# Performance work log

Hardware: AMD Instinct MI355X
Metric: run time of the kernel (lower is better)

The kernel has to match this reference:

```python
import jax, jax.numpy as jnp
import numpy as np

N_NODES = 100000
N_EDGES = 1600000
IN_DIM, HID_DIM, OUT_DIM = 128, 128, 64


def gcn_conv(x, W, b, src, dst, edge_weight, n_nodes):
    """PyG GCNConv: symmetric norm with self-loops (weight 1.0), x@W, scatter-add, +bias."""
    xw = x @ W                                   # [N, out]
    deg = jax.ops.segment_sum(edge_weight, dst, num_segments=n_nodes) + 1.0  # self-loop weight 1
    dis = jnp.where(deg > 0, jax.lax.rsqrt(deg), 0.0)       # deg^{-1/2}
    norm = dis[src] * edge_weight * dis[dst]                # per-edge norm
    agg = jax.ops.segment_sum(norm[:, None] * xw[src], dst, num_segments=n_nodes)
    self_term = (dis * dis)[:, None] * xw                   # self-loop contribution
    return agg + self_term + b


def setup_inputs() -> dict:
    key = jax.random.key(0)
    ks = jax.random.split(key, 12)
    x = jax.random.normal(ks[0], (N_NODES, IN_DIM), dtype=jnp.float32)
    edge_index = jax.random.randint(ks[1], (2, N_EDGES), 0, N_NODES, dtype=jnp.int64 if jax.config.jax_enable_x64 else jnp.int32)
    edge_curvature = jax.random.normal(ks[2], (N_EDGES, 1), dtype=jnp.float32)
    s = 0.1
    W1 = jax.random.normal(ks[3], (IN_DIM, HID_DIM), dtype=jnp.float32) * s
    b1 = jnp.zeros((HID_DIM,), dtype=jnp.float32)
    W2 = jax.random.normal(ks[4], (HID_DIM, OUT_DIM), dtype=jnp.float32) * s
    b2 = jnp.zeros((OUT_DIM,), dtype=jnp.float32)
    mw1 = jax.random.normal(ks[5], (1, 16), dtype=jnp.float32) * s
    mb1 = jnp.zeros((16,), dtype=jnp.float32)
    mw2 = jax.random.normal(ks[6], (16, 1), dtype=jnp.float32) * s
    mb2 = jnp.zeros((1,), dtype=jnp.float32)
    return {"x": x, "edge_index": edge_index, "edge_curvature": edge_curvature,
            "W1": W1, "b1": b1, "W2": W2, "b2": b2,
            "mw1": mw1, "mb1": mb1, "mw2": mw2, "mb2": mb2}


def reference(x, edge_index, edge_curvature, W1, b1, W2, b2, mw1, mb1, mw2, mb2):
    src, dst = edge_index[0], edge_index[1]
    # curv_mlp: Linear(1,16) -> ReLU -> Linear(16,1) -> Sigmoid
    h = jax.nn.relu(edge_curvature @ mw1 + mb1)
    w = jax.nn.sigmoid(h @ mw2 + mb2)[:, 0]
    edge_weight = 0.1 + 0.9 * w
    h1 = jax.nn.relu(gcn_conv(x, W1, b1, src, dst, edge_weight, N_NODES))
    # dropout p=0.5 is identity in eval mode
    out = gcn_conv(h1, W2, b2, src, dst, edge_weight, N_NODES)
    return out
```

## Files before the change

### kernel.cpp

```cpp
#include <hip/hip_runtime.h>


constexpr int N_NODES = 100000;
constexpr int N_EDGES = 1600000;
constexpr int IN_DIM  = 128;
constexpr int HID_DIM = 128;
constexpr int OUT_DIM = 64;

constexpr int RANGE = 256;
constexpr int NBUK  = (N_NODES + RANGE - 1) / RANGE;
constexpr int EPB   = 8192;
constexpr int NPART = (N_EDGES + EPB - 1) / EPB;
constexpr int STAGE_CAP = 6144;

using bf16x8 = __attribute__((ext_vector_type(8))) short;
using f32x4  = __attribute__((ext_vector_type(4))) float;

__device__ __forceinline__ unsigned short f2b(float f)
{
    unsigned int u = __float_as_uint(f);
    u += 0x7fffu + ((u >> 16) & 1u);
    return (unsigned short)(u >> 16);
}

__device__ __forceinline__ float edge_weight_mlp(float c,
                                                 const float* __restrict__ mw1,
                                                 const float* __restrict__ mb1,
                                                 const float* __restrict__ mw2,
                                                 const float* __restrict__ mb2)
{
    float z = mb2[0];
#pragma unroll
    for (int i = 0; i < 16; ++i) {
        float h = fmaf(c, mw1[i], mb1[i]);
        h = fmaxf(h, 0.0f);
        z = fmaf(h, mw2[i], z);
    }
    float s = 1.0f / (1.0f + __expf(-z));
    return fmaf(0.9f, s, 0.1f);
}

__global__ __launch_bounds__(512) void k_hist(const int* __restrict__ dst,
                                              int* __restrict__ blockHist,
                                              int* __restrict__ gcnt)
{
    __shared__ int hist[NBUK];
    const int tid = threadIdx.x;
    const int b   = blockIdx.x;
    for (int i = tid; i < NBUK; i += 512) hist[i] = 0;
    __syncthreads();
    const int base = b * EPB;
    const int n = min(EPB, N_EDGES - base);
    for (int i = tid; i < n; i += 512)
        atomicAdd(&hist[dst[base + i] >> 8], 1);
    __syncthreads();
    for (int i = tid; i < NBUK; i += 512) {
        int h = hist[i];
        blockHist[(size_t)i * NPART + b] = h;
        if (h) atomicAdd(&gcnt[i], h);
    }
}

__global__ __launch_bounds__(512) void k_scan_buckets(const int* __restrict__ gcnt,
                                                      int* __restrict__ bucketBase)
{
    __shared__ int sm[512];
    const int t = threadIdx.x;
    int v = (t < NBUK) ? gcnt[t] : 0;
    sm[t] = v;
    __syncthreads();
#pragma unroll
    for (int o = 1; o < 512; o <<= 1) {
        int u = (t >= o) ? sm[t - o] : 0;
        __syncthreads();
        sm[t] += u;
        __syncthreads();
    }
    if (t < NBUK) bucketBase[t] = sm[t] - v;
    if (t == NBUK - 1) bucketBase[NBUK] = sm[t];
}

__global__ __launch_bounds__(256) void k_colscan(int* __restrict__ blockHist,
                                                 const int* __restrict__ bucketBase)
{
    const int j = blockIdx.x;
    const int t = threadIdx.x;
    __shared__ int sm[256];
    int v = (t < NPART) ? blockHist[(size_t)j * NPART + t] : 0;
    sm[t] = v;
    __syncthreads();
#pragma unroll
    for (int o = 1; o < 256; o <<= 1) {
        int u = (t >= o) ? sm[t - o] : 0;
        __syncthreads();
        sm[t] += u;
        __syncthreads();
    }
    if (t < NPART)
        blockHist[(size_t)j * NPART + t] = bucketBase[j] + sm[t] - v;
}

__global__ __launch_bounds__(512) void k_partition(const float* __restrict__ curv,
                                                   const int*   __restrict__ src,
                                                   const int*   __restrict__ dst,
                                                   const float* __restrict__ mw1,
                                                   const float* __restrict__ mb1,
                                                   const float* __restrict__ mw2,
                                                   const float* __restrict__ mb2,
                                                   const int*   __restrict__ blockHist,
                                                   int2* __restrict__ ep_tmp)
{
    __shared__ int cur[NBUK];
    const int tid = threadIdx.x;
    const int b   = blockIdx.x;
    for (int i = tid; i < NBUK; i += 512)
        cur[i] = blockHist[(size_t)i * NPART + b];
    __syncthreads();
    const int base = b * EPB;
    const int n = min(EPB, N_EDGES - base);
    for (int i = tid; i < n; i += 512) {
        int e = base + i;
        int d = dst[e];
        float w = edge_weight_mlp(curv[e], mw1, mb1, mw2, mb2);
        int pos = atomicAdd(&cur[d >> 8], 1);
        int meta = src[e] | ((d & (RANGE - 1)) << 17);
        ep_tmp[pos] = make_int2(meta, __float_as_int(w));
    }
}

__global__ __launch_bounds__(256) void k_bucket_sort(const int2* __restrict__ ep_tmp,
                                                     const int*  __restrict__ bucketBase,
                                                     int2* __restrict__ ep,
                                                     int*  __restrict__ rp,
                                                     float* __restrict__ dis)
{
    const int b   = blockIdx.x;
    const int tid = threadIdx.x;
    const int base  = bucketBase[b];
    const int nE    = bucketBase[b + 1] - base;
    const int node0 = b * RANGE;
    const int nNodes = min(RANGE, N_NODES - node0);

    __shared__ int2  stage[STAGE_CAP];
    __shared__ int   cnt[RANGE];
    __shared__ float deg[RANGE];
    __shared__ int   sm[RANGE];
    __shared__ int   cur[RANGE];

    const bool fit = (nE <= STAGE_CAP);

    cnt[tid] = 0;
    deg[tid] = 0.0f;
    __syncthreads();
    for (int i = tid; i < nE; i += 256) {
        int2 t = ep_tmp[base + i];
        if (fit) stage[i] = t;
        int dl = (t.x >> 17) & (RANGE - 1);
        atomicAdd(&cnt[dl], 1);
        atomicAdd(&deg[dl], __int_as_float(t.y));
    }
    __syncthreads();
    int c = cnt[tid];
    sm[tid] = c;
    __syncthreads();
#pragma unroll
    for (int o = 1; o < 256; o <<= 1) {
        int u = (tid >= o) ? sm[tid - o] : 0;
        __syncthreads();
        sm[tid] += u;
        __syncthreads();
    }
    int excl = sm[tid] - c;
    cur[tid] = base + excl;
    if (tid < nNodes) {
        rp[node0 + tid]  = base + excl;
        dis[node0 + tid] = rsqrtf(deg[tid] + 1.0f);
    }
    if (b == NBUK - 1 && tid == 0) rp[N_NODES] = N_EDGES;
    __syncthreads();
    for (int i = tid; i < nE; i += 256) {
        int2 t = fit ? stage[i] : ep_tmp[base + i];
        int dl = (t.x >> 17) & (RANGE - 1);
        int pos = atomicAdd(&cur[dl], 1);
        ep[pos] = make_int2(t.x & 0x1FFFF, t.y);
    }
}

template <int KIN, int KOUT>
__global__ __launch_bounds__(256) void k_prepack(const float* __restrict__ W,
                                                 unsigned short* __restrict__ wp)
{
    constexpr int KS = KIN / 32;
    constexpr int NSLOT = (KOUT / 16) * KS * 64;
    int idx = blockIdx.x * blockDim.x + threadIdx.x;
    if (idx >= NSLOT) return;
    int l  = idx & 63;
    int t  = idx >> 6;
    int ks = t % KS;
    int nt = t / KS;
    int col = nt * 16 + (l & 15);
    int k0  = ks * 32 + (l >> 4) * 8;
    unsigned short o[8];
#pragma unroll
    for (int j = 0; j < 8; ++j)
        o[j] = f2b(W[(k0 + j) * KOUT + col]);
    *reinterpret_cast<uint4*>(&wp[(size_t)idx * 8]) = *reinterpret_cast<uint4*>(o);
}

template <int KIN, int KOUT, bool AFP32>
__global__ __launch_bounds__(256) void k_gemm_mfma(const void* __restrict__ Aptr,
                                                   const unsigned short* __restrict__ Wp,
                                                   const float* __restrict__ dis,
                                                   unsigned short* __restrict__ C)
{
    constexpr int NT = KOUT / 16;
    constexpr int KS = KIN / 32;
    const int tid  = threadIdx.x;
    const int lane = tid & 63;
    const int wave = blockIdx.x * (blockDim.x >> 6) + (tid >> 6);
    const int row0 = wave * 16;
    if (row0 >= N_NODES) return;

    f32x4 acc[NT];
#pragma unroll
    for (int nt = 0; nt < NT; ++nt)
        acc[nt] = f32x4{0.f, 0.f, 0.f, 0.f};

    const int arow = row0 + (lane & 15);
    const int koff = (lane >> 4) * 8;
#pragma unroll
    for (int ks = 0; ks < KS; ++ks) {
        bf16x8 a;
        if constexpr (AFP32) {
            const float* A = (const float*)Aptr;
            const float* p = A + (size_t)arow * KIN + ks * 32 + koff;
            float4 f0 = *reinterpret_cast<const float4*>(p);
            float4 f1 = *reinterpret_cast<const float4*>(p + 4);
            a[0] = (short)f2b(f0.x); a[1] = (short)f2b(f0.y);
            a[2] = (short)f2b(f0.z); a[3] = (short)f2b(f0.w);
            a[4] = (short)f2b(f1.x); a[5] = (short)f2b(f1.y);
            a[6] = (short)f2b(f1.z); a[7] = (short)f2b(f1.w);
        } else {
            const unsigned short* A = (const unsigned short*)Aptr;
            a = *reinterpret_cast<const bf16x8*>(A + (size_t)arow * KIN + ks * 32 + koff);
        }
#pragma unroll
        for (int nt = 0; nt < NT; ++nt) {
            bf16x8 bfr = *reinterpret_cast<const bf16x8*>(Wp + ((size_t)(nt * KS + ks) * 64 + lane) * 8);
            acc[nt] = __builtin_amdgcn_mfma_f32_16x16x32_bf16(a, bfr, acc[nt], 0, 0, 0);
        }
    }

    const int r0 = row0 + ((lane >> 4) << 2);
    const int c0 = lane & 15;
    float dv[4];
#pragma unroll
    for (int r = 0; r < 4; ++r) dv[r] = dis[r0 + r];
#pragma unroll
    for (int nt = 0; nt < NT; ++nt) {
#pragma unroll
        for (int r = 0; r < 4; ++r)
            C[(size_t)(r0 + r) * KOUT + nt * 16 + c0] = f2b(acc[nt][r] * dv[r]);
    }
}

template <int DIM, bool RELU, bool OBF16>
__global__ __launch_bounds__(256) void k_gather(const int*  __restrict__ rp,
                                                const int2* __restrict__ ep,
                                                const unsigned short* __restrict__ xws,
                                                const float* __restrict__ dis,
                                                const float* __restrict__ bias,
                                                void* __restrict__ out)
{
    constexpr int TPN = DIM / 8;
    constexpr int NPB = 256 / TPN;
    const int tid = threadIdx.x;
    const int n   = blockIdx.x * NPB + tid / TPN;
    const int d8  = tid % TPN;
    const uint4* xw8 = reinterpret_cast<const uint4*>(xws);
    const int beg = rp[n];
    const int end = rp[n + 1];

    float a0[8] = {0,0,0,0,0,0,0,0};
    float a1[8] = {0,0,0,0,0,0,0,0};

    auto fma8 = [](float w, uint4 u, float* acc) {
        acc[0] = fmaf(w, __uint_as_float(u.x << 16),          acc[0]);
        acc[1] = fmaf(w, __uint_as_float(u.x & 0xFFFF0000u),  acc[1]);
        acc[2] = fmaf(w, __uint_as_float(u.y << 16),          acc[2]);
        acc[3] = fmaf(w, __uint_as_float(u.y & 0xFFFF0000u),  acc[3]);
        acc[4] = fmaf(w, __uint_as_float(u.z << 16),          acc[4]);
        acc[5] = fmaf(w, __uint_as_float(u.z & 0xFFFF0000u),  acc[5]);
        acc[6] = fmaf(w, __uint_as_float(u.w << 16),          acc[6]);
        acc[7] = fmaf(w, __uint_as_float(u.w & 0xFFFF0000u),  acc[7]);
    };

    int i = beg;
    for (; i + 8 <= end; i += 8) {
        int2 e0 = ep[i],     e1 = ep[i + 1], e2 = ep[i + 2], e3 = ep[i + 3];
        int2 e4 = ep[i + 4], e5 = ep[i + 5], e6 = ep[i + 6], e7 = ep[i + 7];
        uint4 u0 = xw8[(size_t)e0.x * TPN + d8];
        uint4 u1 = xw8[(size_t)e1.x * TPN + d8];
        uint4 u2 = xw8[(size_t)e2.x * TPN + d8];
        uint4 u3 = xw8[(size_t)e3.x * TPN + d8];
        uint4 u4 = xw8[(size_t)e4.x * TPN + d8];
        uint4 u5 = xw8[(size_t)e5.x * TPN + d8];
        uint4 u6 = xw8[(size_t)e6.x * TPN + d8];
        uint4 u7 = xw8[(size_t)e7.x * TPN + d8];
        fma8(__int_as_float(e0.y), u0, a0);
        fma8(__int_as_float(e1.y), u1, a1);
        fma8(__int_as_float(e2.y), u2, a0);
        fma8(__int_as_float(e3.y), u3, a1);
        fma8(__int_as_float(e4.y), u4, a0);
        fma8(__int_as_float(e5.y), u5, a1);
        fma8(__int_as_float(e6.y), u6, a0);
        fma8(__int_as_float(e7.y), u7, a1);
    }
    for (; i < end; ++i) {
        int2 e = ep[i];
        uint4 u = xw8[(size_t)e.x * TPN + d8];
        fma8(__int_as_float(e.y), u, a0);
    }
    {
        uint4 un = xw8[(size_t)n * TPN + d8];
        fma8(1.0f, un, a0);
    }

    const float dn = dis[n];
    const float4* b4 = reinterpret_cast<const float4*>(bias);
    float4 blo = b4[d8 * 2];
    float4 bhi = b4[d8 * 2 + 1];
    float v[8];
    v[0] = fmaf(dn, a0[0] + a1[0], blo.x);
    v[1] = fmaf(dn, a0[1] + a1[1], blo.y);
    v[2] = fmaf(dn, a0[2] + a1[2], blo.z);
    v[3] = fmaf(dn, a0[3] + a1[3], blo.w);
    v[4] = fmaf(dn, a0[4] + a1[4], bhi.x);
    v[5] = fmaf(dn, a0[5] + a1[5], bhi.y);
    v[6] = fmaf(dn, a0[6] + a1[6], bhi.z);
    v[7] = fmaf(dn, a0[7] + a1[7], bhi.w);
    if (RELU) {
#pragma unroll
        for (int j = 0; j < 8; ++j) v[j] = fmaxf(v[j], 0.0f);
    }
    if (OBF16) {
        uint4 o;
        o.x = (unsigned)f2b(v[0]) | ((unsigned)f2b(v[1]) << 16);
        o.y = (unsigned)f2b(v[2]) | ((unsigned)f2b(v[3]) << 16);
        o.z = (unsigned)f2b(v[4]) | ((unsigned)f2b(v[5]) << 16);
        o.w = (unsigned)f2b(v[6]) | ((unsigned)f2b(v[7]) << 16);
        reinterpret_cast<uint4*>(out)[(size_t)n * TPN + d8] = o;
    } else {
        float4* o4 = reinterpret_cast<float4*>(out);
        o4[(size_t)n * (DIM / 4) + d8 * 2]     = make_float4(v[0], v[1], v[2], v[3]);
        o4[(size_t)n * (DIM / 4) + d8 * 2 + 1] = make_float4(v[4], v[5], v[6], v[7]);
    }
}

extern "C" void kernel_launch(void* const* d_in, const int* in_sizes, int n_in,
                              void* d_out, int out_size, void* d_ws, size_t ws_size,
                              hipStream_t stream)
{
    const float* x    = (const float*)d_in[0];
    const int*   eidx = (const int*)  d_in[1];
    const float* curv = (const float*)d_in[2];
    const float* W1   = (const float*)d_in[3];
    const float* b1   = (const float*)d_in[4];
    const float* W2   = (const float*)d_in[5];
    const float* b2   = (const float*)d_in[6];
    const float* mw1  = (const float*)d_in[7];
    const float* mb1  = (const float*)d_in[8];
    const float* mw2  = (const float*)d_in[9];
    const float* mb2  = (const float*)d_in[10];

    const int* src = eidx;
    const int* dst = eidx + N_EDGES;
    float* out = (float*)d_out;

    char*  ws  = (char*)d_ws;
    size_t off = 0;
    auto alloc = [&](size_t bytes) -> void* {
        void* p = ws + off;
        off += (bytes + 255) & ~(size_t)255;
        return p;
    };
    float* dis       = (float*)alloc(sizeof(float) * N_NODES);
    int*   rp        = (int*)  alloc(sizeof(int) * (N_NODES + 1));
    int*   gcnt      = (int*)  alloc(sizeof(int) * NBUK);
    int*   bucketBase= (int*)  alloc(sizeof(int) * (NBUK + 1));
    int*   blockHist = (int*)  alloc(sizeof(int) * (size_t)NBUK * NPART);
    int2*  ep_tmp    = (int2*) alloc(sizeof(int2) * N_EDGES);
    int2*  ep        = (int2*) alloc(sizeof(int2) * N_EDGES);
    unsigned short* xws = (unsigned short*)alloc(sizeof(unsigned short) * (size_t)N_NODES * HID_DIM);
    unsigned short* h1b = (unsigned short*)alloc(sizeof(unsigned short) * (size_t)N_NODES * HID_DIM);
    unsigned short* wp1 = (unsigned short*)alloc(sizeof(unsigned short) * (HID_DIM / 16) * (IN_DIM / 32) * 64 * 8);
    unsigned short* wp2 = (unsigned short*)alloc(sizeof(unsigned short) * (OUT_DIM / 16) * (HID_DIM / 32) * 64 * 8);

    hipMemsetAsync(gcnt, 0, sizeof(int) * NBUK, stream);

    const int B = 256;
    auto cdiv = [](long long a, long long b) { return (int)((a + b - 1) / b); };

    k_hist        <<<NPART, 512, 0, stream>>>(dst, blockHist, gcnt);
    k_scan_buckets<<<1, 512, 0, stream>>>(gcnt, bucketBase);
    k_colscan     <<<NBUK, 256, 0, stream>>>(blockHist, bucketBase);
    k_partition   <<<NPART, 512, 0, stream>>>(curv, src, dst, mw1, mb1, mw2, mb2,
                                              blockHist, ep_tmp);
    k_bucket_sort <<<NBUK, 256, 0, stream>>>(ep_tmp, bucketBase, ep, rp, dis);

    k_prepack<IN_DIM, HID_DIM><<<cdiv((HID_DIM/16)*(IN_DIM/32)*64, B), B, 0, stream>>>(W1, wp1);
    k_prepack<HID_DIM, OUT_DIM><<<cdiv((OUT_DIM/16)*(HID_DIM/32)*64, B), B, 0, stream>>>(W2, wp2);

    const int GEMM_GRID = cdiv(N_NODES / 16, 4);

    k_gemm_mfma<IN_DIM, HID_DIM, true><<<GEMM_GRID, 256, 0, stream>>>(x, wp1, dis, xws);
    k_gather<HID_DIM, true, true><<<N_NODES / 16, 256, 0, stream>>>(rp, ep, xws, dis, b1, h1b);

    k_gemm_mfma<HID_DIM, OUT_DIM, false><<<GEMM_GRID, 256, 0, stream>>>(h1b, wp2, dis, xws);
    k_gather<OUT_DIM, false, false><<<N_NODES / 32, 256, 0, stream>>>(rp, ep, xws, dis, b2, out);
}
```

Baseline: 209.8 us.

## Sort nodes by in-degree so gather blocks process similar-degree nodes

Adds a counting sort of nodes by in-degree (histogram, scan, placement) and has both gather kernels look up their node through this permutation. Nodes in the same wavefront then have similar edge counts, which is meant to cut load imbalance and divergence in the per-node edge loops. The cost is three extra small kernel launches plus an indirection. Output writes become scattered, and the node order inside each degree bin is nondeterministic.

Measured after the change: 213.4 us. Within noise of the previous version (+1.7%).

```diff
diff --git a/kernel.cpp b/kernel.cpp
--- a/kernel.cpp
+++ b/kernel.cpp
@@ -12,6 +12,7 @@
 constexpr int EPB   = 8192;
 constexpr int NPART = (N_EDGES + EPB - 1) / EPB;
 constexpr int STAGE_CAP = 6144;
+constexpr int DBINS = 128;
 
 using bf16x8 = __attribute__((ext_vector_type(8))) short;
 using f32x4  = __attribute__((ext_vector_type(4))) float;
@@ -183,6 +184,68 @@
         int dl = (t.x >> 17) & (RANGE - 1);
         int pos = atomicAdd(&cur[dl], 1);
         ep[pos] = make_int2(t.x & 0x1FFFF, t.y);
+    }
+}
+
+__global__ __launch_bounds__(256) void k_deghist(const int* __restrict__ rp,
+                                                 int* __restrict__ dhist)
+{
+    __shared__ int h[DBINS];
+    const int tid = threadIdx.x;
+    if (tid < DBINS) h[tid] = 0;
+    __syncthreads();
+    int n = blockIdx.x * 256 + tid;
+    if (n < N_NODES) {
+        int d = min(rp[n + 1] - rp[n], DBINS - 1);
+        atomicAdd(&h[d], 1);
+    }
+    __syncthreads();
+    if (tid < DBINS && h[tid]) atomicAdd(&dhist[tid], h[tid]);
+}
+
+__global__ __launch_bounds__(128) void k_degscan(const int* __restrict__ dhist,
+                                                 int* __restrict__ dbase)
+{
+    __shared__ int sm[DBINS];
+    const int t = threadIdx.x;
+    int v = dhist[t];
+    sm[t] = v;
+    __syncthreads();
+#pragma unroll
+    for (int o = 1; o < DBINS; o <<= 1) {
+        int u = (t >= o) ? sm[t - o] : 0;
+        __syncthreads();
+        sm[t] += u;
+        __syncthreads();
+    }
+    dbase[t] = sm[t] - v;
+}
+
+__global__ __launch_bounds__(256) void k_degplace(const int* __restrict__ rp,
+                                                  int* __restrict__ dbase,
+                                                  int* __restrict__ perm)
+{
+    __shared__ int h[DBINS];
+    __shared__ int base[DBINS];
+    __shared__ int cur[DBINS];
+    const int tid = threadIdx.x;
+    if (tid < DBINS) h[tid] = 0;
+    __syncthreads();
+    int n = blockIdx.x * 256 + tid;
+    int bin = -1;
+    if (n < N_NODES) {
+        bin = min(rp[n + 1] - rp[n], DBINS - 1);
+        atomicAdd(&h[bin], 1);
+    }
+    __syncthreads();
+    if (tid < DBINS) {
+        base[tid] = h[tid] ? atomicAdd(&dbase[tid], h[tid]) : 0;
+        cur[tid] = 0;
+    }
+    __syncthreads();
+    if (n < N_NODES) {
+        int off = atomicAdd(&cur[bin], 1);
+        perm[base[bin] + off] = n;
     }
 }
 
@@ -265,7 +328,8 @@
 }
 
 template <int DIM, bool RELU, bool OBF16>
-__global__ __launch_bounds__(256) void k_gather(const int*  __restrict__ rp,
+__global__ __launch_bounds__(256) void k_gather(const int*  __restrict__ perm,
+                                                const int*  __restrict__ rp,
                                                 const int2* __restrict__ ep,
                                                 const unsigned short* __restrict__ xws,
                                                 const float* __restrict__ dis,
@@ -275,7 +339,7 @@
     constexpr int TPN = DIM / 8;
     constexpr int NPB = 256 / TPN;
     const int tid = threadIdx.x;
-    const int n   = blockIdx.x * NPB + tid / TPN;
+    const int n   = perm[blockIdx.x * NPB + tid / TPN];
     const int d8  = tid % TPN;
     const uint4* xw8 = reinterpret_cast<const uint4*>(xws);
     const int beg = rp[n];
@@ -387,6 +451,9 @@
     float* dis       = (float*)alloc(sizeof(float) * N_NODES);
     int*   rp        = (int*)  alloc(sizeof(int) * (N_NODES + 1));
     int*   gcnt      = (int*)  alloc(sizeof(int) * NBUK);
+    int*   dhist     = (int*)  alloc(sizeof(int) * DBINS);
+    int*   dbase     = (int*)  alloc(sizeof(int) * DBINS);
+    int*   perm      = (int*)  alloc(sizeof(int) * N_NODES);
     int*   bucketBase= (int*)  alloc(sizeof(int) * (NBUK + 1));
     int*   blockHist = (int*)  alloc(sizeof(int) * (size_t)NBUK * NPART);
     int2*  ep_tmp    = (int2*) alloc(sizeof(int2) * N_EDGES);
@@ -396,7 +463,7 @@
     unsigned short* wp1 = (unsigned short*)alloc(sizeof(unsigned short) * (HID_DIM / 16) * (IN_DIM / 32) * 64 * 8);
     unsigned short* wp2 = (unsigned short*)alloc(sizeof(unsigned short) * (OUT_DIM / 16) * (HID_DIM / 32) * 64 * 8);
 
-    hipMemsetAsync(gcnt, 0, sizeof(int) * NBUK, stream);
+    hipMemsetAsync(gcnt, 0, (size_t)((char*)dbase - (char*)gcnt), stream);
 
     const int B = 256;
     auto cdiv = [](long long a, long long b) { return (int)((a + b - 1) / b); };
@@ -408,14 +475,18 @@
                                               blockHist, ep_tmp);
     k_bucket_sort <<<NBUK, 256, 0, stream>>>(ep_tmp, bucketBase, ep, rp, dis);
 
+    k_deghist <<<cdiv(N_NODES, 256), 256, 0, stream>>>(rp, dhist);
+    k_degscan <<<1, DBINS, 0, stream>>>(dhist, dbase);
+    k_degplace<<<cdiv(N_NODES, 256), 256, 0, stream>>>(rp, dbase, perm);
+
     k_prepack<IN_DIM, HID_DIM><<<cdiv((HID_DIM/16)*(IN_DIM/32)*64, B), B, 0, stream>>>(W1, wp1);
     k_prepack<HID_DIM, OUT_DIM><<<cdiv((OUT_DIM/16)*(HID_DIM/32)*64, B), B, 0, stream>>>(W2, wp2);
 
     const int GEMM_GRID = cdiv(N_NODES / 16, 4);
 
     k_gemm_mfma<IN_DIM, HID_DIM, true><<<GEMM_GRID, 256, 0, stream>>>(x, wp1, dis, xws);
-    k_gather<HID_DIM, true, true><<<N_NODES / 16, 256, 0, stream>>>(rp, ep, xws, dis, b1, h1b);
+    k_gather<HID_DIM, true, true><<<N_NODES / 16, 256, 0, stream>>>(perm, rp, ep, xws, dis, b1, h1b);
 
     k_gemm_mfma<HID_DIM, OUT_DIM, false><<<GEMM_GRID, 256, 0, stream>>>(h1b, wp2, dis, xws);
-    k_gather<OUT_DIM, false, false><<<N_NODES / 32, 256, 0, stream>>>(rp, ep, xws, dis, b2, out);
-}
+    k_gather<OUT_DIM, false, false><<<N_NODES / 32, 256, 0, stream>>>(perm, rp, ep, xws, dis, b2, out);
+}
```

## Sort nodes by degree within windows to balance gather wavefronts

Applied to the files above, without the earlier changes.

Adds a kernel that counting-sorts nodes by in-degree inside windows of 2048 nodes and writes a permutation. Both gather kernels then process nodes in this permuted order, so nodes of similar degree share a wavefront and lanes spend less time idle on divergent loop trip counts. The cost is an extra small kernel launch, an indirect index load per thread, and scattered output row writes that lose some coalescing.

Result: no change. 208.2 us, median of 2 (-0.8%).

```diff
diff --git a/kernel.cpp b/kernel.cpp
--- a/kernel.cpp
+++ b/kernel.cpp
@@ -12,6 +12,8 @@
 constexpr int EPB   = 8192;
 constexpr int NPART = (N_EDGES + EPB - 1) / EPB;
 constexpr int STAGE_CAP = 6144;
+constexpr int WSIZE = 2048;
+constexpr int WBINS = 64;
 
 using bf16x8 = __attribute__((ext_vector_type(8))) short;
 using f32x4  = __attribute__((ext_vector_type(4))) float;
@@ -183,6 +185,50 @@
         int dl = (t.x >> 17) & (RANGE - 1);
         int pos = atomicAdd(&cur[dl], 1);
         ep[pos] = make_int2(t.x & 0x1FFFF, t.y);
+    }
+}
+
+__global__ __launch_bounds__(256) void k_wsort(const int* __restrict__ rp,
+                                               int* __restrict__ perm)
+{
+    const int w    = blockIdx.x;
+    const int tid  = threadIdx.x;
+    const int node0 = w * WSIZE;
+    const int nN   = min(WSIZE, N_NODES - node0);
+
+    __shared__ int h[WBINS];
+    __shared__ int base[WBINS];
+    __shared__ int cur[WBINS];
+    if (tid < WBINS) h[tid] = 0;
+    __syncthreads();
+
+    int mybin[WSIZE / 256];
+#pragma unroll
+    for (int j = 0; j < WSIZE / 256; ++j) {
+        int li = tid + j * 256;
+        int b = -1;
+        if (li < nN) {
+            int n = node0 + li;
+            b = min(rp[n + 1] - rp[n], WBINS - 1);
+            atomicAdd(&h[b], 1);
+        }
+        mybin[j] = b;
+    }
+    __syncthreads();
+    if (tid < WBINS) {
+        int s = 0;
+        for (int i = 0; i < tid; ++i) s += h[i];
+        base[tid] = s;
+        cur[tid]  = 0;
+    }
+    __syncthreads();
+#pragma unroll
+    for (int j = 0; j < WSIZE / 256; ++j) {
+        int b = mybin[j];
+        if (b >= 0) {
+            int off = atomicAdd(&cur[b], 1);
+            perm[node0 + base[b] + off] = node0 + tid + j * 256;
+        }
     }
 }
 
@@ -265,7 +311,8 @@
 }
 
 template <int DIM, bool RELU, bool OBF16>
-__global__ __launch_bounds__(256) void k_gather(const int*  __restrict__ rp,
+__global__ __launch_bounds__(256) void k_gather(const int*  __restrict__ perm,
+                                                const int*  __restrict__ rp,
                                                 const int2* __restrict__ ep,
                                                 const unsigned short* __restrict__ xws,
                                                 const float* __restrict__ dis,
@@ -275,7 +322,7 @@
     constexpr int TPN = DIM / 8;
     constexpr int NPB = 256 / TPN;
     const int tid = threadIdx.x;
-    const int n   = blockIdx.x * NPB + tid / TPN;
+    const int n   = perm[blockIdx.x * NPB + tid / TPN];
     const int d8  = tid % TPN;
     const uint4* xw8 = reinterpret_cast<const uint4*>(xws);
     const int beg = rp[n];
@@ -387,6 +434,7 @@
     float* dis       = (float*)alloc(sizeof(float) * N_NODES);
     int*   rp        = (int*)  alloc(sizeof(int) * (N_NODES + 1));
     int*   gcnt      = (int*)  alloc(sizeof(int) * NBUK);
+    int*   perm      = (int*)  alloc(sizeof(int) * N_NODES);
     int*   bucketBase= (int*)  alloc(sizeof(int) * (NBUK + 1));
     int*   blockHist = (int*)  alloc(sizeof(int) * (size_t)NBUK * NPART);
     int2*  ep_tmp    = (int2*) alloc(sizeof(int2) * N_EDGES);
@@ -408,14 +456,16 @@
                                               blockHist, ep_tmp);
     k_bucket_sort <<<NBUK, 256, 0, stream>>>(ep_tmp, bucketBase, ep, rp, dis);
 
+    k_wsort<<<cdiv(N_NODES, WSIZE), 256, 0, stream>>>(rp, perm);
+
     k_prepack<IN_DIM, HID_DIM><<<cdiv((HID_DIM/16)*(IN_DIM/32)*64, B), B, 0, stream>>>(W1, wp1);
     k_prepack<HID_DIM, OUT_DIM><<<cdiv((OUT_DIM/16)*(HID_DIM/32)*64, B), B, 0, stream>>>(W2, wp2);
 
     const int GEMM_GRID = cdiv(N_NODES / 16, 4);
 
     k_gemm_mfma<IN_DIM, HID_DIM, true><<<GEMM_GRID, 256, 0, stream>>>(x, wp1, dis, xws);
-    k_gather<HID_DIM, true, true><<<N_NODES / 16, 256, 0, stream>>>(rp, ep, xws, dis, b1, h1b);
+    k_gather<HID_DIM, true, true><<<N_NODES / 16, 256, 0, stream>>>(perm, rp, ep, xws, dis, b1, h1b);
 
     k_gemm_mfma<HID_DIM, OUT_DIM, false><<<GEMM_GRID, 256, 0, stream>>>(h1b, wp2, dis, xws);
-    k_gather<OUT_DIM, false, false><<<N_NODES / 32, 256, 0, stream>>>(rp, ep, xws, dis, b2, out);
-}
+    k_gather<OUT_DIM, false, false><<<N_NODES / 32, 256, 0, stream>>>(perm, rp, ep, xws, dis, b2, out);
+}
```

## Sort nodes by degree within buckets and prefetch edge batches in gather

Applied to the files above, without the earlier changes.

The bucket sort kernel now builds a per-bucket permutation that groups nodes by in-degree using a small shared-memory counting sort. The gather kernels process nodes in that order so that nodes with similar edge counts share a wavefront, which reduces divergence and idle lanes. The gather loop also software-pipelines the edge-index loads by fetching the next 8 edges before issuing the feature gathers for the current 8. This costs an extra permutation read, scattered output writes and more registers per thread.

New measurement: 221.7 us. +5.6%, slower.

```diff
diff --git a/kernel.cpp b/kernel.cpp
--- a/kernel.cpp
+++ b/kernel.cpp
@@ -12,6 +12,7 @@
 constexpr int EPB   = 8192;
 constexpr int NPART = (N_EDGES + EPB - 1) / EPB;
 constexpr int STAGE_CAP = 6144;
+constexpr int DB = 64;
 
 using bf16x8 = __attribute__((ext_vector_type(8))) short;
 using f32x4  = __attribute__((ext_vector_type(4))) float;
@@ -132,7 +133,8 @@
                                                      const int*  __restrict__ bucketBase,
                                                      int2* __restrict__ ep,
                                                      int*  __restrict__ rp,
-                                                     float* __restrict__ dis)
+                                                     float* __restrict__ dis,
+                                                     int*  __restrict__ perm)
 {
     const int b   = blockIdx.x;
     const int tid = threadIdx.x;
@@ -146,11 +148,15 @@
     __shared__ float deg[RANGE];
     __shared__ int   sm[RANGE];
     __shared__ int   cur[RANGE];
+    __shared__ int   dbh[DB];
+    __shared__ int   dbb[DB];
+    __shared__ int   dbc[DB];
 
     const bool fit = (nE <= STAGE_CAP);
 
     cnt[tid] = 0;
     deg[tid] = 0.0f;
+    if (tid < DB) { dbh[tid] = 0; dbc[tid] = 0; }
     __syncthreads();
     for (int i = tid; i < nE; i += 256) {
         int2 t = ep_tmp[base + i];
@@ -172,12 +178,25 @@
     }
     int excl = sm[tid] - c;
     cur[tid] = base + excl;
+    int bin = -1;
     if (tid < nNodes) {
         rp[node0 + tid]  = base + excl;
         dis[node0 + tid] = rsqrtf(deg[tid] + 1.0f);
+        bin = min(c, DB - 1);
+        atomicAdd(&dbh[bin], 1);
     }
     if (b == NBUK - 1 && tid == 0) rp[N_NODES] = N_EDGES;
     __syncthreads();
+    if (tid == 0) {
+        int run = 0;
+#pragma unroll
+        for (int j = 0; j < DB; ++j) { dbb[j] = run; run += dbh[j]; }
+    }
+    __syncthreads();
+    if (tid < nNodes) {
+        int off = atomicAdd(&dbc[bin], 1);
+        perm[node0 + dbb[bin] + off] = node0 + tid;
+    }
     for (int i = tid; i < nE; i += 256) {
         int2 t = fit ? stage[i] : ep_tmp[base + i];
         int dl = (t.x >> 17) & (RANGE - 1);
@@ -265,7 +284,8 @@
 }
 
 template <int DIM, bool RELU, bool OBF16>
-__global__ __launch_bounds__(256) void k_gather(const int*  __restrict__ rp,
+__global__ __launch_bounds__(256) void k_gather(const int*  __restrict__ perm,
+                                                const int*  __restrict__ rp,
                                                 const int2* __restrict__ ep,
                                                 const unsigned short* __restrict__ xws,
                                                 const float* __restrict__ dis,
@@ -275,7 +295,7 @@
     constexpr int TPN = DIM / 8;
     constexpr int NPB = 256 / TPN;
     const int tid = threadIdx.x;
-    const int n   = blockIdx.x * NPB + tid / TPN;
+    const int n   = perm[blockIdx.x * NPB + tid / TPN];
     const int d8  = tid % TPN;
     const uint4* xw8 = reinterpret_cast<const uint4*>(xws);
     const int beg = rp[n];
@@ -296,25 +316,40 @@
     };
 
     int i = beg;
-    for (; i + 8 <= end; i += 8) {
-        int2 e0 = ep[i],     e1 = ep[i + 1], e2 = ep[i + 2], e3 = ep[i + 3];
-        int2 e4 = ep[i + 4], e5 = ep[i + 5], e6 = ep[i + 6], e7 = ep[i + 7];
-        uint4 u0 = xw8[(size_t)e0.x * TPN + d8];
-        uint4 u1 = xw8[(size_t)e1.x * TPN + d8];
-        uint4 u2 = xw8[(size_t)e2.x * TPN + d8];
-        uint4 u3 = xw8[(size_t)e3.x * TPN + d8];
-        uint4 u4 = xw8[(size_t)e4.x * TPN + d8];
-        uint4 u5 = xw8[(size_t)e5.x * TPN + d8];
-        uint4 u6 = xw8[(size_t)e6.x * TPN + d8];
-        uint4 u7 = xw8[(size_t)e7.x * TPN + d8];
-        fma8(__int_as_float(e0.y), u0, a0);
-        fma8(__int_as_float(e1.y), u1, a1);
-        fma8(__int_as_float(e2.y), u2, a0);
-        fma8(__int_as_float(e3.y), u3, a1);
-        fma8(__int_as_float(e4.y), u4, a0);
-        fma8(__int_as_float(e5.y), u5, a1);
-        fma8(__int_as_float(e6.y), u6, a0);
-        fma8(__int_as_float(e7.y), u7, a1);
+    int2 c0, c1, c2, c3, c4, c5, c6, c7;
+    bool have = (i + 8 <= end);
+    if (have) {
+        c0 = ep[i];     c1 = ep[i + 1]; c2 = ep[i + 2]; c3 = ep[i + 3];
+        c4 = ep[i + 4]; c5 = ep[i + 5]; c6 = ep[i + 6]; c7 = ep[i + 7];
+    }
+    while (have) {
+        const int ni = i + 8;
+        const bool nhave = (ni + 8 <= end);
+        int2 n0, n1, n2, n3, n4, n5, n6, n7;
+        if (nhave) {
+            n0 = ep[ni];     n1 = ep[ni + 1]; n2 = ep[ni + 2]; n3 = ep[ni + 3];
+            n4 = ep[ni + 4]; n5 = ep[ni + 5]; n6 = ep[ni + 6]; n7 = ep[ni + 7];
+        }
+        uint4 u0 = xw8[(size_t)c0.x * TPN + d8];
+        uint4 u1 = xw8[(size_t)c1.x * TPN + d8];
+        uint4 u2 = xw8[(size_t)c2.x * TPN + d8];
+        uint4 u3 = xw8[(size_t)c3.x * TPN + d8];
+        uint4 u4 = xw8[(size_t)c4.x * TPN + d8];
+        uint4 u5 = xw8[(size_t)c5.x * TPN + d8];
+        uint4 u6 = xw8[(size_t)c6.x * TPN + d8];
+        uint4 u7 = xw8[(size_t)c7.x * TPN + d8];
+        fma8(__int_as_float(c0.y), u0, a0);
+        fma8(__int_as_float(c1.y), u1, a1);
+        fma8(__int_as_float(c2.y), u2, a0);
+        fma8(__int_as_float(c3.y), u3, a1);
+        fma8(__int_as_float(c4.y), u4, a0);
+        fma8(__int_as_float(c5.y), u5, a1);
+        fma8(__int_as_float(c6.y), u6, a0);
+        fma8(__int_as_float(c7.y), u7, a1);
+        c0 = n0; c1 = n1; c2 = n2; c3 = n3;
+        c4 = n4; c5 = n5; c6 = n6; c7 = n7;
+        i = ni;
+        have = nhave;
     }
     for (; i < end; ++i) {
         int2 e = ep[i];
@@ -387,6 +422,7 @@
     float* dis       = (float*)alloc(sizeof(float) * N_NODES);
     int*   rp        = (int*)  alloc(sizeof(int) * (N_NODES + 1));
     int*   gcnt      = (int*)  alloc(sizeof(int) * NBUK);
+    int*   perm      = (int*)  alloc(sizeof(int) * N_NODES);
     int*   bucketBase= (int*)  alloc(sizeof(int) * (NBUK + 1));
     int*   blockHist = (int*)  alloc(sizeof(int) * (size_t)NBUK * NPART);
     int2*  ep_tmp    = (int2*) alloc(sizeof(int2) * N_EDGES);
@@ -406,7 +442,7 @@
     k_colscan     <<<NBUK, 256, 0, stream>>>(blockHist, bucketBase);
     k_partition   <<<NPART, 512, 0, stream>>>(curv, src, dst, mw1, mb1, mw2, mb2,
                                               blockHist, ep_tmp);
-    k_bucket_sort <<<NBUK, 256, 0, stream>>>(ep_tmp, bucketBase, ep, rp, dis);
+    k_bucket_sort <<<NBUK, 256, 0, stream>>>(ep_tmp, bucketBase, ep, rp, dis, perm);
 
     k_prepack<IN_DIM, HID_DIM><<<cdiv((HID_DIM/16)*(IN_DIM/32)*64, B), B, 0, stream>>>(W1, wp1);
     k_prepack<HID_DIM, OUT_DIM><<<cdiv((OUT_DIM/16)*(HID_DIM/32)*64, B), B, 0, stream>>>(W2, wp2);
@@ -414,8 +450,8 @@
     const int GEMM_GRID = cdiv(N_NODES / 16, 4);
 
     k_gemm_mfma<IN_DIM, HID_DIM, true><<<GEMM_GRID, 256, 0, stream>>>(x, wp1, dis, xws);
-    k_gather<HID_DIM, true, true><<<N_NODES / 16, 256, 0, stream>>>(rp, ep, xws, dis, b1, h1b);
+    k_gather<HID_DIM, true, true><<<N_NODES / 16, 256, 0, stream>>>(perm, rp, ep, xws, dis, b1, h1b);
 
     k_gemm_mfma<HID_DIM, OUT_DIM, false><<<GEMM_GRID, 256, 0, stream>>>(h1b, wp2, dis, xws);
-    k_gather<OUT_DIM, false, false><<<N_NODES / 32, 256, 0, stream>>>(rp, ep, xws, dis, b2, out);
-}
+    k_gather<OUT_DIM, false, false><<<N_NODES / 32, 256, 0, stream>>>(perm, rp, ep, xws, dis, b2, out);
+}
```
